# Optimization experiments

Measured on AMD Instinct MI355X. Metric: run time of the kernel, lower is better.

Reference implementation:

```python
import jax, jax.numpy as jnp
import numpy as np

N_NODES = 100000
N_EDGES = 1600000
N_GRAPHS = 128
H = 64          # hidden_channels_gin
L = 3           # num_layers
IN_X = 4
IN_E = 8
G_DIM = H * L   # pooled concat dim = hidden_channels_global
OUT = 1


def _w(k, shape):
    return (jax.random.normal(k, shape, jnp.float32) * 0.1)


def setup_inputs() -> dict:
    key = jax.random.key(0)
    ks = jax.random.split(key, 24)
    inp = {
        'x': jax.random.normal(ks[0], (N_NODES, IN_X), jnp.float32),
        'edge_index': jax.random.randint(ks[1], (2, N_EDGES), 0, N_NODES),
        'batch': jnp.sort(jax.random.randint(ks[2], (N_NODES,), 0, N_GRAPHS)),
        'edge_attr': jax.random.normal(ks[3], (N_EDGES, IN_E), jnp.float32),
        # node embedding MLP (MLPembd: Linear-ReLU-Linear-ReLU-Linear)
        'nW1': _w(ks[4], (IN_X, H)), 'nb1': jnp.zeros((H,), jnp.float32),
        'nW2': _w(ks[5], (H, H)),    'nb2': jnp.zeros((H,), jnp.float32),
        'nW3': _w(ks[6], (H, H)),    'nb3': jnp.zeros((H,), jnp.float32),
        # edge embedding MLP (gin_MLP_layers[0])
        'eW1': _w(ks[7], (IN_E, H)), 'eb1': jnp.zeros((H,), jnp.float32),
        'eW2': _w(ks[8], (H, H)),    'eb2': jnp.zeros((H,), jnp.float32),
        'eW3': _w(ks[9], (H, H)),    'eb3': jnp.zeros((H,), jnp.float32),
        # GINE layers: trainable eps + 2-layer MLP nn per layer (stacked over L)
        'gine_eps': jnp.zeros((L,), jnp.float32),
        'gW1': _w(ks[10], (L, H, H)), 'gb1': jnp.zeros((L, H), jnp.float32),
        'gW2': _w(ks[11], (L, H, H)), 'gb2': jnp.zeros((L, H), jnp.float32),
        # output MLP: Linear - BN(eval) - LeakyReLU - (Dropout eval) - Linear
        'oW1': _w(ks[12], (G_DIM, G_DIM)), 'ob1': jnp.zeros((G_DIM,), jnp.float32),
        'ogamma': jnp.ones((G_DIM,), jnp.float32), 'obeta': jnp.zeros((G_DIM,), jnp.float32),
        'oW2': _w(ks[13], (G_DIM, OUT)), 'ob2': jnp.zeros((OUT,), jnp.float32),
    }
    return inp


def _mlp3(x, W1, b1, W2, b2, W3, b3):
    x = jax.nn.relu(x @ W1 + b1)
    x = jax.nn.relu(x @ W2 + b2)
    return x @ W3 + b3


def _forward(x, edge_index, batch, edge_attr,
             nW1, nb1, nW2, nb2, nW3, nb3,
             eW1, eb1, eW2, eb2, eW3, eb3,
             gine_eps, gW1, gb1, gW2, gb2,
             oW1, ob1, ogamma, obeta, oW2, ob2):
    src, dst = edge_index[0], edge_index[1]
    h = _mlp3(x, nW1, nb1, nW2, nb2, nW3, nb3)                    # [N, H]
    ea = _mlp3(edge_attr, eW1, eb1, eW2, eb2, eW3, eb3)           # [E, H]
    pooled = []
    for l in range(L):  # fixed small layer count
        msg = jax.nn.leaky_relu(h[src] + ea)                      # [E, H] gather + add
        agg = jax.ops.segment_max(msg, dst, num_segments=N_NODES) # max aggregation
        agg = jnp.where(jnp.isfinite(agg), agg, 0.0)              # isolated nodes -> 0
        z = (1.0 + gine_eps[l]) * h + agg
        h = jax.nn.leaky_relu(z @ gW1[l] + gb1[l]) @ gW2[l] + gb2[l]
        pooled.append(jax.ops.segment_max(h, batch, num_segments=N_GRAPHS))
    hp = jnp.concatenate(pooled, axis=1)                          # [G, H*L]
    y = hp @ oW1 + ob1
    y = ogamma * y + obeta            # eval-mode BatchNorm1d (running mean=0, var=1)
    y = jax.nn.leaky_relu(y)          # Dropout inactive at inference
    logits = y @ oW2 + ob2            # [G, 1]
    return logits, jax.nn.sigmoid(logits)


def reference(x, edge_index, batch, edge_attr,
              nW1, nb1, nW2, nb2, nW3, nb3,
              eW1, eb1, eW2, eb2, eW3, eb3,
              gine_eps, gW1, gb1, gW2, gb2,
              oW1, ob1, ogamma, obeta, oW2, ob2):
    return _forward(x, edge_index, batch, edge_attr,
                    nW1, nb1, nW2, nb2, nW3, nb3,
                    eW1, eb1, eW2, eb2, eW3, eb3,
                    gine_eps, gW1, gb1, gW2, gb2,
                    oW1, ob1, ogamma, obeta, oW2, ob2)
```

## Files before the change

### kernel.cpp

```cpp
#include <hip/hip_runtime.h>
#include <hip/hip_bf16.h>

#define LRELU(x) ((x) > 0.0f ? (x) : 0.01f * (x))

typedef __attribute__((ext_vector_type(4))) short bf16x4;
typedef __attribute__((ext_vector_type(4))) float f32x4;

__device__ __forceinline__ unsigned fenc(float f) {
    unsigned u = __float_as_uint(f);
    return (u & 0x80000000u) ? ~u : (u | 0x80000000u);
}
__device__ __forceinline__ float fdec(unsigned u) {
    return (u & 0x80000000u) ? __uint_as_float(u & 0x7fffffffu) : __uint_as_float(~u);
}
__device__ __forceinline__ short f2bf(float f) {
    __hip_bfloat16 b = __float2bfloat16(f);
    return *reinterpret_cast<short*>(&b);
}
__device__ __forceinline__ float bf2f(short s) {
    return __uint_as_float(((unsigned)(unsigned short)s) << 16);
}

__device__ __forceinline__ f32x4 mfma16(bf16x4 a, bf16x4 b, f32x4 c) {
#if __has_builtin(__builtin_amdgcn_mfma_f32_16x16x16bf16_1k)
    return __builtin_amdgcn_mfma_f32_16x16x16bf16_1k(a, b, c, 0, 0, 0);
#else
    asm("v_mfma_f32_16x16x16_bf16 %0, %1, %2, %0" : "+v"(c) : "v"(a), "v"(b));
    return c;
#endif
}

__global__ __launch_bounds__(256) void hist_kernel(const int* __restrict__ ei,
                                                   int* __restrict__ deg_p,
                                                   int* __restrict__ rank, int E)
{
    const int stride = gridDim.x * blockDim.x * 4;
    const bool vec = ((E & 3) == 0);
    for (int e4 = (blockIdx.x * blockDim.x + threadIdx.x) * 4; e4 < E; e4 += stride) {
        if (vec && e4 + 3 < E) {
            const int4 d = *reinterpret_cast<const int4*>(ei + E + e4);
            int4 r;
            r.x = atomicAdd(&deg_p[(size_t)d.x * 4], 1);
            r.y = atomicAdd(&deg_p[(size_t)d.y * 4], 1);
            r.z = atomicAdd(&deg_p[(size_t)d.z * 4], 1);
            r.w = atomicAdd(&deg_p[(size_t)d.w * 4], 1);
            *reinterpret_cast<int4*>(rank + e4) = r;
        } else {
            for (int k = 0; k < 4 && e4 + k < E; ++k) {
                const int d = ei[E + e4 + k];
                rank[e4 + k] = atomicAdd(&deg_p[(size_t)d * 4], 1);
            }
        }
    }
}

__global__ __launch_bounds__(1024) void scan_kernel(const int* __restrict__ deg_p,
                                                    int* __restrict__ rowptr, int N)
{
    __shared__ int wsum[16];
    __shared__ int tiletot;
    const int lane = threadIdx.x & 63;
    const int w    = threadIdx.x >> 6;
    int carry = 0;
    for (int base = 0; base < N; base += 4096) {
        const int i = base + (int)threadIdx.x * 4;
        int4 v = {0, 0, 0, 0};
        if (i < N)     v.x = deg_p[(size_t)i * 4];
        if (i + 1 < N) v.y = deg_p[(size_t)(i + 1) * 4];
        if (i + 2 < N) v.z = deg_p[(size_t)(i + 2) * 4];
        if (i + 3 < N) v.w = deg_p[(size_t)(i + 3) * 4];
        const int tot = v.x + v.y + v.z + v.w;
        int s = tot;
#pragma unroll
        for (int off = 1; off < 64; off <<= 1) {
            int t = __shfl_up(s, off);
            if (lane >= off) s += t;
        }
        if (lane == 63) wsum[w] = s;
        __syncthreads();
        if (threadIdx.x == 0) {
            int acc = 0;
#pragma unroll
            for (int k = 0; k < 16; ++k) { int t = wsum[k]; wsum[k] = acc; acc += t; }
            tiletot = acc;
        }
        __syncthreads();
        const int excl = carry + wsum[w] + (s - tot);
        int4 o;
        o.x = excl; o.y = excl + v.x; o.z = o.y + v.y; o.w = o.z + v.z;
        if (i + 3 < N) {
            *reinterpret_cast<int4*>(rowptr + i) = o;
        } else {
            if (i < N)     rowptr[i] = o.x;
            if (i + 1 < N) rowptr[i + 1] = o.y;
            if (i + 2 < N) rowptr[i + 2] = o.z;
        }
        carry += tiletot;
        __syncthreads();
    }
    if (threadIdx.x == 0) rowptr[N] = carry;
}

__global__ __launch_bounds__(256) void scatter_kernel(
    const int* __restrict__ ei, const int* __restrict__ rank,
    const int* __restrict__ rowptr, int2* __restrict__ pack, int E)
{
    const int stride = gridDim.x * blockDim.x * 4;
    const bool vec = ((E & 3) == 0);
    for (int e4 = (blockIdx.x * blockDim.x + threadIdx.x) * 4; e4 < E; e4 += stride) {
        if (vec && e4 + 3 < E) {
            const int4 s  = *reinterpret_cast<const int4*>(ei + e4);
            const int4 d  = *reinterpret_cast<const int4*>(ei + E + e4);
            const int4 rk = *reinterpret_cast<const int4*>(rank + e4);
            pack[rowptr[d.x] + rk.x] = make_int2(s.x, e4 + 0);
            pack[rowptr[d.y] + rk.y] = make_int2(s.y, e4 + 1);
            pack[rowptr[d.z] + rk.z] = make_int2(s.z, e4 + 2);
            pack[rowptr[d.w] + rk.w] = make_int2(s.w, e4 + 3);
        } else {
            for (int k = 0; k < 4 && e4 + k < E; ++k) {
                const int e = e4 + k;
                pack[rowptr[ei[E + e]] + rank[e]] = make_int2(ei[e], e);
            }
        }
    }
}

__global__ __launch_bounds__(256) void edge_mlp_mfma(
    const float* __restrict__ eattr, const int2* __restrict__ pack,
    const float* __restrict__ W1, const float* __restrict__ b1,
    const float* __restrict__ W2, const float* __restrict__ b2,
    const float* __restrict__ W3, const float* __restrict__ b3,
    short* __restrict__ eout, int E)
{
    const int lane = threadIdx.x & 63;
    const int el   = lane & 15;
    const int g    = lane >> 4;

    bf16x4 w1f[4];
    bf16x4 w2f[4][4];
    bf16x4 w3f[4][4];
    f32x4  bf1[4], bf2[4], bf3[4];
#pragma unroll
    for (int t = 0; t < 4; ++t) {
        const int c = t * 16 + el;
#pragma unroll
        for (int j = 0; j < 4; ++j) {
            const int k = g * 4 + j;
            w1f[t][j] = (k < 8) ? f2bf(W1[k * 64 + c]) : (short)0;
        }
#pragma unroll
        for (int kb = 0; kb < 4; ++kb) {
#pragma unroll
            for (int j = 0; j < 4; ++j) {
                const int k = kb * 16 + g * 4 + j;
                w2f[t][kb][j] = f2bf(W2[k * 64 + c]);
                w3f[t][kb][j] = f2bf(W3[k * 64 + c]);
            }
        }
        const float4 v1 = *reinterpret_cast<const float4*>(b1 + t * 16 + g * 4);
        const float4 v2 = *reinterpret_cast<const float4*>(b2 + t * 16 + g * 4);
        const float4 v3 = *reinterpret_cast<const float4*>(b3 + t * 16 + g * 4);
        bf1[t][0] = v1.x; bf1[t][1] = v1.y; bf1[t][2] = v1.z; bf1[t][3] = v1.w;
        bf2[t][0] = v2.x; bf2[t][1] = v2.y; bf2[t][2] = v2.z; bf2[t][3] = v2.w;
        bf3[t][0] = v3.x; bf3[t][1] = v3.y; bf3[t][2] = v3.z; bf3[t][3] = v3.w;
    }

    const int nblk = (E + 15) >> 4;
    const int wid  = (int)((blockIdx.x * blockDim.x + threadIdx.x) >> 6);
    const int nw   = (int)((gridDim.x * blockDim.x) >> 6);

    for (int eb = wid; eb < nblk; eb += nw) {
        const int e  = eb * 16 + el;
        const int ec = min(e, E - 1);
        const int eid = pack[ec].y;

        bf16x4 bfr = (bf16x4)0;
        if (g < 2) {
            const float4 av = *reinterpret_cast<const float4*>(eattr + (size_t)eid * 8 + g * 4);
            bfr[0] = f2bf(av.x); bfr[1] = f2bf(av.y);
            bfr[2] = f2bf(av.z); bfr[3] = f2bf(av.w);
        }

        f32x4  acc[4];
        bf16x4 act[4];

#pragma unroll
        for (int t = 0; t < 4; ++t) acc[t] = mfma16(w1f[t], bfr, bf1[t]);
#pragma unroll
        for (int t = 0; t < 4; ++t)
#pragma unroll
            for (int j = 0; j < 4; ++j) act[t][j] = f2bf(fmaxf(acc[t][j], 0.0f));

#pragma unroll
        for (int t = 0; t < 4; ++t) {
            f32x4 a = bf2[t];
#pragma unroll
            for (int kb = 0; kb < 4; ++kb) a = mfma16(w2f[t][kb], act[kb], a);
            acc[t] = a;
        }
#pragma unroll
        for (int t = 0; t < 4; ++t)
#pragma unroll
            for (int j = 0; j < 4; ++j) act[t][j] = f2bf(fmaxf(acc[t][j], 0.0f));

#pragma unroll
        for (int t = 0; t < 4; ++t) {
            f32x4 a = bf3[t];
#pragma unroll
            for (int kb = 0; kb < 4; ++kb) a = mfma16(w3f[t][kb], act[kb], a);
            bf16x4 o;
#pragma unroll
            for (int j = 0; j < 4; ++j) o[j] = f2bf(a[j]);
            if (e < E)
                *reinterpret_cast<bf16x4*>(eout + (size_t)e * 64 + t * 16 + g * 4) = o;
        }
    }
}

__global__ __launch_bounds__(256) void node_mlp_mfma(
    const float* __restrict__ x,
    const float* __restrict__ W1, const float* __restrict__ b1,
    const float* __restrict__ W2, const float* __restrict__ b2,
    const float* __restrict__ W3, const float* __restrict__ b3,
    short* __restrict__ hout, int N)
{
    const int lane = threadIdx.x & 63;
    const int el   = lane & 15;
    const int g    = lane >> 4;

    bf16x4 w1f[4];
    bf16x4 w2f[4][4];
    bf16x4 w3f[4][4];
    f32x4  bf1[4], bf2[4], bf3[4];
#pragma unroll
    for (int t = 0; t < 4; ++t) {
        const int c = t * 16 + el;
#pragma unroll
        for (int j = 0; j < 4; ++j) {
            const int k = g * 4 + j;
            w1f[t][j] = (k < 4) ? f2bf(W1[k * 64 + c]) : (short)0;
        }
#pragma unroll
        for (int kb = 0; kb < 4; ++kb) {
#pragma unroll
            for (int j = 0; j < 4; ++j) {
                const int k = kb * 16 + g * 4 + j;
                w2f[t][kb][j] = f2bf(W2[k * 64 + c]);
                w3f[t][kb][j] = f2bf(W3[k * 64 + c]);
            }
        }
        const float4 v1 = *reinterpret_cast<const float4*>(b1 + t * 16 + g * 4);
        const float4 v2 = *reinterpret_cast<const float4*>(b2 + t * 16 + g * 4);
        const float4 v3 = *reinterpret_cast<const float4*>(b3 + t * 16 + g * 4);
        bf1[t][0] = v1.x; bf1[t][1] = v1.y; bf1[t][2] = v1.z; bf1[t][3] = v1.w;
        bf2[t][0] = v2.x; bf2[t][1] = v2.y; bf2[t][2] = v2.z; bf2[t][3] = v2.w;
        bf3[t][0] = v3.x; bf3[t][1] = v3.y; bf3[t][2] = v3.z; bf3[t][3] = v3.w;
    }

    const int nblk = (N + 15) >> 4;
    const int wid  = (int)((blockIdx.x * blockDim.x + threadIdx.x) >> 6);
    const int nw   = (int)((gridDim.x * blockDim.x) >> 6);

    for (int nb = wid; nb < nblk; nb += nw) {
        const int n  = nb * 16 + el;
        const int nc = min(n, N - 1);

        bf16x4 bfr = (bf16x4)0;
        if (g == 0) {
            const float4 xv = *reinterpret_cast<const float4*>(x + (size_t)nc * 4);
            bfr[0] = f2bf(xv.x); bfr[1] = f2bf(xv.y);
            bfr[2] = f2bf(xv.z); bfr[3] = f2bf(xv.w);
        }

        f32x4  acc[4];
        bf16x4 act[4];
#pragma unroll
        for (int t = 0; t < 4; ++t) acc[t] = mfma16(w1f[t], bfr, bf1[t]);
#pragma unroll
        for (int t = 0; t < 4; ++t)
#pragma unroll
            for (int j = 0; j < 4; ++j) act[t][j] = f2bf(fmaxf(acc[t][j], 0.0f));

#pragma unroll
        for (int t = 0; t < 4; ++t) {
            f32x4 a = bf2[t];
#pragma unroll
            for (int kb = 0; kb < 4; ++kb) a = mfma16(w2f[t][kb], act[kb], a);
            acc[t] = a;
        }
#pragma unroll
        for (int t = 0; t < 4; ++t)
#pragma unroll
            for (int j = 0; j < 4; ++j) act[t][j] = f2bf(fmaxf(acc[t][j], 0.0f));

#pragma unroll
        for (int t = 0; t < 4; ++t) {
            f32x4 a = bf3[t];
#pragma unroll
            for (int kb = 0; kb < 4; ++kb) a = mfma16(w3f[t][kb], act[kb], a);
            bf16x4 o;
#pragma unroll
            for (int j = 0; j < 4; ++j) o[j] = f2bf(a[j]);
            if (n < N)
                *reinterpret_cast<bf16x4*>(hout + (size_t)n * 64 + t * 16 + g * 4) = o;
        }
    }
}

__global__ __launch_bounds__(256) void agg_kernel(
    const short* __restrict__ h_in, short* __restrict__ z_out,
    const int* __restrict__ rowptr, const int2* __restrict__ pack,
    const short* __restrict__ ea,
    const float* __restrict__ geps, int l, int N)
{
    const int lane = threadIdx.x & 63;
    const int g    = lane >> 4;
    const int el   = lane & 15;
    const float ope = 1.0f + geps[l];

    const int nwave = gridDim.x * 4;
    const int w     = blockIdx.x * 4 + (threadIdx.x >> 6);
    const int chunk = (N + nwave - 1) / nwave;
    const int n0 = w * chunk;
    const int n1 = min(N, n0 + chunk);
    if (n0 >= n1) return;

    int r0 = rowptr[n0];
    for (int n = n0; n < n1; ++n) {
        const int r1 = rowptr[n + 1];

        float m0 = -INFINITY, m1 = -INFINITY, m2 = -INFINITY, m3 = -INFINITY;
        for (int r = r0; r < r1; r += 16) {
#pragma unroll
            for (int u = 0; u < 4; ++u) {
                const int rc = min(r + u * 4 + g, r1 - 1);
                const int s  = pack[rc].x;
                const bf16x4 hv = *reinterpret_cast<const bf16x4*>(h_in + (size_t)s * 64 + el * 4);
                const bf16x4 ev = *reinterpret_cast<const bf16x4*>(ea + (size_t)rc * 64 + el * 4);
                float c0 = bf2f(hv[0]) + bf2f(ev[0]);
                float c1 = bf2f(hv[1]) + bf2f(ev[1]);
                float c2 = bf2f(hv[2]) + bf2f(ev[2]);
                float c3 = bf2f(hv[3]) + bf2f(ev[3]);
                c0 = LRELU(c0); c1 = LRELU(c1); c2 = LRELU(c2); c3 = LRELU(c3);
                m0 = fmaxf(m0, c0); m1 = fmaxf(m1, c1);
                m2 = fmaxf(m2, c2); m3 = fmaxf(m3, c3);
            }
        }
        m0 = fmaxf(m0, __shfl_xor(m0, 16)); m0 = fmaxf(m0, __shfl_xor(m0, 32));
        m1 = fmaxf(m1, __shfl_xor(m1, 16)); m1 = fmaxf(m1, __shfl_xor(m1, 32));
        m2 = fmaxf(m2, __shfl_xor(m2, 16)); m2 = fmaxf(m2, __shfl_xor(m2, 32));
        m3 = fmaxf(m3, __shfl_xor(m3, 16)); m3 = fmaxf(m3, __shfl_xor(m3, 32));

        if (g == 0) {
            const bf16x4 hn = *reinterpret_cast<const bf16x4*>(h_in + (size_t)n * 64 + el * 4);
            bf16x4 zo;
            zo[0] = f2bf(ope * bf2f(hn[0]) + ((m0 == -INFINITY) ? 0.0f : m0));
            zo[1] = f2bf(ope * bf2f(hn[1]) + ((m1 == -INFINITY) ? 0.0f : m1));
            zo[2] = f2bf(ope * bf2f(hn[2]) + ((m2 == -INFINITY) ? 0.0f : m2));
            zo[3] = f2bf(ope * bf2f(hn[3]) + ((m3 == -INFINITY) ? 0.0f : m3));
            *reinterpret_cast<bf16x4*>(z_out + (size_t)n * 64 + el * 4) = zo;
        }
        r0 = r1;
    }
}

__global__ __launch_bounds__(256) void mlp_pool_kernel(
    const short* __restrict__ z, short* __restrict__ h_out,
    const int* __restrict__ batch,
    const float* __restrict__ gW1, const float* __restrict__ gb1,
    const float* __restrict__ gW2, const float* __restrict__ gb2,
    unsigned* __restrict__ pooled, int l, int N)
{
    const int lane = threadIdx.x & 63;
    const int el   = lane & 15;
    const int g    = lane >> 4;

    const float* W1 = gW1 + (size_t)l * 4096;
    const float* W2 = gW2 + (size_t)l * 4096;
    bf16x4 w1f[4][4], w2f[4][4];
    f32x4  bA[4], bB[4];
#pragma unroll
    for (int t = 0; t < 4; ++t) {
        const int c = t * 16 + el;
#pragma unroll
        for (int kb = 0; kb < 4; ++kb) {
#pragma unroll
            for (int j = 0; j < 4; ++j) {
                const int k = kb * 16 + g * 4 + j;
                w1f[t][kb][j] = f2bf(W1[k * 64 + c]);
                w2f[t][kb][j] = f2bf(W2[k * 64 + c]);
            }
        }
        const float4 v1 = *reinterpret_cast<const float4*>(gb1 + l * 64 + t * 16 + g * 4);
        const float4 v2 = *reinterpret_cast<const float4*>(gb2 + l * 64 + t * 16 + g * 4);
        bA[t][0] = v1.x; bA[t][1] = v1.y; bA[t][2] = v1.z; bA[t][3] = v1.w;
        bB[t][0] = v2.x; bB[t][1] = v2.y; bB[t][2] = v2.z; bB[t][3] = v2.w;
    }

    const int nblk = (N + 15) >> 4;
    const int wid  = (int)((blockIdx.x * blockDim.x + threadIdx.x) >> 6);
    const int nw   = (int)((gridDim.x * blockDim.x) >> 6);

    for (int nb = wid; nb < nblk; nb += nw) {
        const int n  = nb * 16 + el;
        const bool valid = (n < N);
        const int nc = valid ? n : (N - 1);

        bf16x4 zf[4];
#pragma unroll
        for (int kb = 0; kb < 4; ++kb)
            zf[kb] = *reinterpret_cast<const bf16x4*>(z + (size_t)nc * 64 + kb * 16 + g * 4);

        f32x4  acc[4];
        bf16x4 act[4];
#pragma unroll
        for (int t = 0; t < 4; ++t) {
            f32x4 a = bA[t];
#pragma unroll
            for (int kb = 0; kb < 4; ++kb) a = mfma16(w1f[t][kb], zf[kb], a);
            acc[t] = a;
        }
#pragma unroll
        for (int t = 0; t < 4; ++t)
#pragma unroll
            for (int j = 0; j < 4; ++j) act[t][j] = f2bf(LRELU(acc[t][j]));

#pragma unroll
        for (int t = 0; t < 4; ++t) {
            f32x4 a = bB[t];
#pragma unroll
            for (int kb = 0; kb < 4; ++kb) a = mfma16(w2f[t][kb], act[kb], a);
            acc[t] = a;
        }

#pragma unroll
        for (int t = 0; t < 4; ++t) {
            bf16x4 o;
#pragma unroll
            for (int j = 0; j < 4; ++j) o[j] = f2bf(acc[t][j]);
            if (valid)
                *reinterpret_cast<bf16x4*>(h_out + (size_t)n * 64 + t * 16 + g * 4) = o;
        }

        const int gbl = batch[nc];
        const int gb_first = __shfl(gbl, 0);
        const int gb_last  = __shfl(gbl, 15);
        if (gb_first == gb_last) {
#pragma unroll
            for (int t = 0; t < 4; ++t) {
#pragma unroll
                for (int j = 0; j < 4; ++j) {
                    float v = valid ? acc[t][j] : -INFINITY;
                    v = fmaxf(v, __shfl_xor(v, 1));
                    v = fmaxf(v, __shfl_xor(v, 2));
                    v = fmaxf(v, __shfl_xor(v, 4));
                    v = fmaxf(v, __shfl_xor(v, 8));
                    if (el == 0)
                        atomicMax(&pooled[gb_first * 192 + l * 64 + t * 16 + g * 4 + j], fenc(v));
                }
            }
        } else if (valid) {
#pragma unroll
            for (int t = 0; t < 4; ++t)
#pragma unroll
                for (int j = 0; j < 4; ++j)
                    atomicMax(&pooled[gbl * 192 + l * 64 + t * 16 + g * 4 + j], fenc(acc[t][j]));
        }
    }
}

__global__ __launch_bounds__(192) void out_kernel(
    const unsigned* __restrict__ pooled,
    const float* __restrict__ oW1, const float* __restrict__ ob1,
    const float* __restrict__ ogamma, const float* __restrict__ obeta,
    const float* __restrict__ oW2, const float* __restrict__ ob2,
    float* __restrict__ out)
{
    __shared__ float hp[192];
    __shared__ float partial[3];
    const int c = threadIdx.x;
    const int g = blockIdx.x;

    const unsigned u = pooled[g * 192 + c];
    hp[c] = (u == 0u) ? -INFINITY : fdec(u);
    __syncthreads();

    float y = ob1[c];
#pragma unroll 4
    for (int k = 0; k < 192; ++k)
        y += hp[k] * oW1[k * 192 + c];
    y = ogamma[c] * y + obeta[c];
    y = LRELU(y);
    float contrib = y * oW2[c];

#pragma unroll
    for (int off = 32; off > 0; off >>= 1)
        contrib += __shfl_xor(contrib, off);
    if ((threadIdx.x & 63) == 0) partial[threadIdx.x >> 6] = contrib;
    __syncthreads();
    if (threadIdx.x == 0) {
        const float logit = partial[0] + partial[1] + partial[2] + ob2[0];
        out[g] = logit;
        out[128 + g] = 1.0f / (1.0f + expf(-logit));
    }
}

extern "C" void kernel_launch(void* const* d_in, const int* in_sizes, int n_in,
                              void* d_out, int out_size, void* d_ws, size_t ws_size,
                              hipStream_t stream)
{
    const float* x     = (const float*)d_in[0];
    const int*   ei    = (const int*)d_in[1];
    const int*   batch = (const int*)d_in[2];
    const float* eattr = (const float*)d_in[3];
    const float* nW1 = (const float*)d_in[4],  *nb1 = (const float*)d_in[5];
    const float* nW2 = (const float*)d_in[6],  *nb2 = (const float*)d_in[7];
    const float* nW3 = (const float*)d_in[8],  *nb3 = (const float*)d_in[9];
    const float* eW1 = (const float*)d_in[10], *eb1 = (const float*)d_in[11];
    const float* eW2 = (const float*)d_in[12], *eb2 = (const float*)d_in[13];
    const float* eW3 = (const float*)d_in[14], *eb3 = (const float*)d_in[15];
    const float* geps = (const float*)d_in[16];
    const float* gW1 = (const float*)d_in[17], *gb1 = (const float*)d_in[18];
    const float* gW2 = (const float*)d_in[19], *gb2 = (const float*)d_in[20];
    const float* oW1 = (const float*)d_in[21], *ob1 = (const float*)d_in[22];
    const float* ogamma = (const float*)d_in[23], *obeta = (const float*)d_in[24];
    const float* oW2 = (const float*)d_in[25], *ob2 = (const float*)d_in[26];
    float* out = (float*)d_out;

    const int N = in_sizes[0] / 4;
    const int E = in_sizes[3] / 8;
    const size_t EP = ((size_t)E + 15) & ~(size_t)15;

    char* ws = (char*)d_ws;
    size_t off = 0;
    auto take = [&](size_t bytes) { char* p = ws + off; off += (bytes + 255) & ~(size_t)255; return p; };
    short*    ea     = (short*)take(EP * 64 * sizeof(short));
    short*    h0     = (short*)take((size_t)N * 64 * sizeof(short));
    short*    h1     = (short*)take((size_t)N * 64 * sizeof(short));
    int2*     pack   = (int2*)take((size_t)E * sizeof(int2));
    short*    zbuf   = (short*)take((size_t)N * 64 * sizeof(short));
    int*      rank   = (int*)take((size_t)E * sizeof(int));
    int*      rowptr = (int*)take(((size_t)N + 1) * sizeof(int));
    unsigned* pooled = (unsigned*)take(128 * 192 * sizeof(unsigned));
    int* deg_p = (int*)h1;
    (void)ws_size;

    hipMemsetAsync(pooled, 0, 128 * 192 * sizeof(unsigned), stream);
    hipMemsetAsync(deg_p, 0, (size_t)N * 4 * sizeof(int), stream);

    const int gEdge = (E / 4 + 255) / 256 + 1;
    hist_kernel<<<gEdge, 256, 0, stream>>>(ei, deg_p, rank, E);
    scan_kernel<<<1, 1024, 0, stream>>>(deg_p, rowptr, N);
    node_mlp_mfma<<<1024, 256, 0, stream>>>(x, nW1, nb1, nW2, nb2, nW3, nb3, h0, N);
    scatter_kernel<<<gEdge, 256, 0, stream>>>(ei, rank, rowptr, pack, E);
    edge_mlp_mfma<<<2048, 256, 0, stream>>>(eattr, pack, eW1, eb1, eW2, eb2, eW3, eb3, ea, E);

    for (int l = 0; l < 3; ++l) {
        const short* hi = (l & 1) ? h1 : h0;
        short*       ho = (l & 1) ? h0 : h1;
        agg_kernel<<<2048, 256, 0, stream>>>(hi, zbuf, rowptr, pack, ea, geps, l, N);
        mlp_pool_kernel<<<1024, 256, 0, stream>>>(zbuf, ho, batch,
                                                  gW1, gb1, gW2, gb2, pooled, l, N);
    }

    out_kernel<<<128, 192, 0, stream>>>(pooled, oW1, ob1, ogamma, obeta, oW2, ob2, out);
}
```

Before: 713.9 us.

## Pad degree counters, prefetch edge attributes, and shuffle-broadcast neighbor indices

Three changes. First, the per-node degree counters move from a 16-byte to a 64-byte stride, which cuts cache-line sharing between atomics but enlarges the memset and the strided scan reads. Second, the edge MLP software-prefetches the next iteration's edge attributes so the gather latency overlaps the MFMA chain. Third, the aggregation kernel loads 64 neighbor source indices once per wave and broadcasts them with shuffles, replacing the repeated per-lane pack loads inside the inner loop.

```diff
diff --git a/kernel.cpp b/kernel.cpp
--- a/kernel.cpp
+++ b/kernel.cpp
@@ -40,15 +40,15 @@
         if (vec && e4 + 3 < E) {
             const int4 d = *reinterpret_cast<const int4*>(ei + E + e4);
             int4 r;
-            r.x = atomicAdd(&deg_p[(size_t)d.x * 4], 1);
-            r.y = atomicAdd(&deg_p[(size_t)d.y * 4], 1);
-            r.z = atomicAdd(&deg_p[(size_t)d.z * 4], 1);
-            r.w = atomicAdd(&deg_p[(size_t)d.w * 4], 1);
+            r.x = atomicAdd(&deg_p[(size_t)d.x * 16], 1);
+            r.y = atomicAdd(&deg_p[(size_t)d.y * 16], 1);
+            r.z = atomicAdd(&deg_p[(size_t)d.z * 16], 1);
+            r.w = atomicAdd(&deg_p[(size_t)d.w * 16], 1);
             *reinterpret_cast<int4*>(rank + e4) = r;
         } else {
             for (int k = 0; k < 4 && e4 + k < E; ++k) {
                 const int d = ei[E + e4 + k];
-                rank[e4 + k] = atomicAdd(&deg_p[(size_t)d * 4], 1);
+                rank[e4 + k] = atomicAdd(&deg_p[(size_t)d * 16], 1);
             }
         }
     }
@@ -65,10 +65,10 @@
     for (int base = 0; base < N; base += 4096) {
         const int i = base + (int)threadIdx.x * 4;
         int4 v = {0, 0, 0, 0};
-        if (i < N)     v.x = deg_p[(size_t)i * 4];
-        if (i + 1 < N) v.y = deg_p[(size_t)(i + 1) * 4];
-        if (i + 2 < N) v.z = deg_p[(size_t)(i + 2) * 4];
-        if (i + 3 < N) v.w = deg_p[(size_t)(i + 3) * 4];
+        if (i < N)     v.x = deg_p[(size_t)i * 16];
+        if (i + 1 < N) v.y = deg_p[(size_t)(i + 1) * 16];
+        if (i + 2 < N) v.z = deg_p[(size_t)(i + 2) * 16];
+        if (i + 3 < N) v.w = deg_p[(size_t)(i + 3) * 16];
         const int tot = v.x + v.y + v.z + v.w;
         int s = tot;
 #pragma unroll
@@ -168,17 +168,30 @@
     const int nblk = (E + 15) >> 4;
     const int wid  = (int)((blockIdx.x * blockDim.x + threadIdx.x) >> 6);
     const int nw   = (int)((gridDim.x * blockDim.x) >> 6);
+    if (wid >= nblk) return;
+
+    float4 av_cur = {0.f, 0.f, 0.f, 0.f};
+    {
+        const int ec = min(wid * 16 + el, E - 1);
+        const int eid = pack[ec].y;
+        if (g < 2)
+            av_cur = *reinterpret_cast<const float4*>(eattr + (size_t)eid * 8 + g * 4);
+    }
 
     for (int eb = wid; eb < nblk; eb += nw) {
-        const int e  = eb * 16 + el;
-        const int ec = min(e, E - 1);
-        const int eid = pack[ec].y;
+        float4 av_nxt = {0.f, 0.f, 0.f, 0.f};
+        const int ebn = eb + nw;
+        if (ebn < nblk) {
+            const int ecn = min(ebn * 16 + el, E - 1);
+            const int eidn = pack[ecn].y;
+            if (g < 2)
+                av_nxt = *reinterpret_cast<const float4*>(eattr + (size_t)eidn * 8 + g * 4);
+        }
 
         bf16x4 bfr = (bf16x4)0;
         if (g < 2) {
-            const float4 av = *reinterpret_cast<const float4*>(eattr + (size_t)eid * 8 + g * 4);
-            bfr[0] = f2bf(av.x); bfr[1] = f2bf(av.y);
-            bfr[2] = f2bf(av.z); bfr[3] = f2bf(av.w);
+            bfr[0] = f2bf(av_cur.x); bfr[1] = f2bf(av_cur.y);
+            bfr[2] = f2bf(av_cur.z); bfr[3] = f2bf(av_cur.w);
         }
 
         f32x4  acc[4];
@@ -203,6 +216,7 @@
 #pragma unroll
             for (int j = 0; j < 4; ++j) act[t][j] = f2bf(fmaxf(acc[t][j], 0.0f));
 
+        const int e = eb * 16 + el;
 #pragma unroll
         for (int t = 0; t < 4; ++t) {
             f32x4 a = bf3[t];
@@ -214,6 +228,7 @@
             if (e < E)
                 *reinterpret_cast<bf16x4*>(eout + (size_t)e * 64 + t * 16 + g * 4) = o;
         }
+        av_cur = av_nxt;
     }
 }
 
@@ -330,20 +345,24 @@
         const int r1 = rowptr[n + 1];
 
         float m0 = -INFINITY, m1 = -INFINITY, m2 = -INFINITY, m3 = -INFINITY;
-        for (int r = r0; r < r1; r += 16) {
-#pragma unroll
-            for (int u = 0; u < 4; ++u) {
-                const int rc = min(r + u * 4 + g, r1 - 1);
-                const int s  = pack[rc].x;
-                const bf16x4 hv = *reinterpret_cast<const bf16x4*>(h_in + (size_t)s * 64 + el * 4);
-                const bf16x4 ev = *reinterpret_cast<const bf16x4*>(ea + (size_t)rc * 64 + el * 4);
-                float c0 = bf2f(hv[0]) + bf2f(ev[0]);
-                float c1 = bf2f(hv[1]) + bf2f(ev[1]);
-                float c2 = bf2f(hv[2]) + bf2f(ev[2]);
-                float c3 = bf2f(hv[3]) + bf2f(ev[3]);
-                c0 = LRELU(c0); c1 = LRELU(c1); c2 = LRELU(c2); c3 = LRELU(c3);
-                m0 = fmaxf(m0, c0); m1 = fmaxf(m1, c1);
-                m2 = fmaxf(m2, c2); m3 = fmaxf(m3, c3);
+        for (int rb = r0; rb < r1; rb += 64) {
+            const int sv = pack[min(rb + lane, r1 - 1)].x;
+            const int lim = min(r1, rb + 64);
+            for (int rq = rb; rq < lim; rq += 16) {
+#pragma unroll
+                for (int u = 0; u < 4; ++u) {
+                    const int rc = min(rq + u * 4 + g, r1 - 1);
+                    const int s  = __shfl(sv, rc - rb);
+                    const bf16x4 hv = *reinterpret_cast<const bf16x4*>(h_in + (size_t)s * 64 + el * 4);
+                    const bf16x4 ev = *reinterpret_cast<const bf16x4*>(ea + (size_t)rc * 64 + el * 4);
+                    float c0 = bf2f(hv[0]) + bf2f(ev[0]);
+                    float c1 = bf2f(hv[1]) + bf2f(ev[1]);
+                    float c2 = bf2f(hv[2]) + bf2f(ev[2]);
+                    float c3 = bf2f(hv[3]) + bf2f(ev[3]);
+                    c0 = LRELU(c0); c1 = LRELU(c1); c2 = LRELU(c2); c3 = LRELU(c3);
+                    m0 = fmaxf(m0, c0); m1 = fmaxf(m1, c1);
+                    m2 = fmaxf(m2, c2); m3 = fmaxf(m3, c3);
+                }
             }
         }
         m0 = fmaxf(m0, __shfl_xor(m0, 16)); m0 = fmaxf(m0, __shfl_xor(m0, 32));
@@ -546,7 +565,7 @@
     (void)ws_size;
 
     hipMemsetAsync(pooled, 0, 128 * 192 * sizeof(unsigned), stream);
-    hipMemsetAsync(deg_p, 0, (size_t)N * 4 * sizeof(int), stream);
+    hipMemsetAsync(deg_p, 0, (size_t)N * 16 * sizeof(int), stream);
 
     const int gEdge = (E / 4 + 255) / 256 + 1;
     hist_kernel<<<gEdge, 256, 0, stream>>>(ei, deg_p, rank, E);
```

Result: slower. 755.8 us (+5.9%).
